# Optimization experiments

Hardware: AMD Instinct MI355X
Metric: run time of the kernel (lower is better)

## Reference

```python
import jax, jax.numpy as jnp
import numpy as np

N_NODES = 100000
N_EDGES = 1600000
IN_FEATS = 128
OUT_FEATS = 64
NUM_HEADS = 1
K_HOPS = 3
NEG_SLOPE = 0.2


def setup_inputs() -> dict:
    key = jax.random.key(0)
    kf, kw, kl, kr, ks, kd = jax.random.split(key, 6)
    feat = jax.random.normal(kf, (N_NODES, IN_FEATS), dtype=jnp.float32)
    # xavier-normal-ish scaling (gain for relu ~ sqrt(2))
    W = jax.random.normal(kw, (OUT_FEATS * NUM_HEADS, IN_FEATS), dtype=jnp.float32) * np.sqrt(2.0 / (IN_FEATS + OUT_FEATS * NUM_HEADS))
    attn_l = jax.random.normal(kl, (1, NUM_HEADS, OUT_FEATS), dtype=jnp.float32) * 0.1
    attn_r = jax.random.normal(kr, (1, NUM_HEADS, OUT_FEATS), dtype=jnp.float32) * 0.1
    src = jax.random.randint(ks, (N_EDGES,), 0, N_NODES, dtype=jnp.int32)
    dst = jax.random.randint(kd, (N_EDGES,), 0, N_NODES, dtype=jnp.int32)
    return {"feat": feat, "W": W, "attn_l": attn_l, "attn_r": attn_r, "src": src, "dst": dst}


def _edge_softmax(e, dst, n_nodes):
    # e: [E, H, 1]; softmax over incoming edges of each dst node
    emax = jax.ops.segment_max(e, dst, num_segments=n_nodes)  # [N, H, 1]
    ee = jnp.exp(e - emax[dst])
    denom = jax.ops.segment_sum(ee, dst, num_segments=n_nodes)
    return ee / denom[dst]


def reference(feat, W, attn_l, attn_r, src, dst):
    n = feat.shape[0]
    h = (feat @ W.T).reshape(n, NUM_HEADS, OUT_FEATS)  # [N, H, F]
    el = jnp.sum(h * attn_l, axis=-1, keepdims=True)   # [N, H, 1]
    er = jnp.sum(h * attn_r, axis=-1, keepdims=True)   # [N, H, 1]
    e = el[src] + er[dst]                               # [E, H, 1]
    e = jnp.where(e > 0, e, NEG_SLOPE * e)              # leaky_relu
    a = _edge_softmax(e, dst, n)                        # [E, H, 1]

    ones = jnp.ones((src.shape[0],), dtype=feat.dtype)
    out_deg = jax.ops.segment_sum(ones, src, num_segments=n)
    in_deg = jax.ops.segment_sum(ones, dst, num_segments=n)
    out_norm = jnp.power(jnp.clip(out_deg, 1.0, None), -0.5)[:, None, None]  # deg^-0.5
    in_norm = jnp.power(jnp.clip(in_deg, 1.0, None), 0.5)[:, None, None]     # deg^+0.5 (as in source)

    feat_src = h
    for _ in range(K_HOPS):
        feat_src = feat_src * out_norm
        m = feat_src[src] * a                            # [E, H, F]
        feat_src = jax.ops.segment_sum(m, dst, num_segments=n)
        feat_src = feat_src * in_norm
    return feat_src  # [N, H, F]
```

## Files before the change

kernel.cpp:

```cpp
#include <hip/hip_runtime.h>
#include <hip/hip_fp16.h>
#include <math.h>

#define N_NODES 100000
#define N_EDGES 1600000
#define IN_F 128
#define OUT_F 64
#define NEG_SLOPE 0.2f

#define NBUCK 391
#define PB 512
#define EPB (N_EDGES / PB)

#define FS 132

typedef __attribute__((ext_vector_type(8))) short short8;
typedef __attribute__((ext_vector_type(4))) float f32x4;

__device__ __forceinline__ unsigned pack_bf(float f) {
    unsigned u  = __float_as_uint(f);
    unsigned hi = u & 0xffff0000u;
    float    lo = f - __uint_as_float(hi);
    return hi | (__float_as_uint(lo) >> 16);
}

__device__ __forceinline__ void unpack8(uint4 p0, uint4 p1, short8& hi, short8& lo) {
    hi[0] = (short)(p0.x >> 16); lo[0] = (short)(p0.x & 0xffffu);
    hi[1] = (short)(p0.y >> 16); lo[1] = (short)(p0.y & 0xffffu);
    hi[2] = (short)(p0.z >> 16); lo[2] = (short)(p0.z & 0xffffu);
    hi[3] = (short)(p0.w >> 16); lo[3] = (short)(p0.w & 0xffffu);
    hi[4] = (short)(p1.x >> 16); lo[4] = (short)(p1.x & 0xffffu);
    hi[5] = (short)(p1.y >> 16); lo[5] = (short)(p1.y & 0xffffu);
    hi[6] = (short)(p1.z >> 16); lo[6] = (short)(p1.z & 0xffffu);
    hi[7] = (short)(p1.w >> 16); lo[7] = (short)(p1.w & 0xffffu);
}

__global__ __launch_bounds__(256) void k_gemm(
        const float* __restrict__ feat, const float* __restrict__ W,
        const float* __restrict__ attn_l, const float* __restrict__ attn_r,
        __half* __restrict__ h16, float* __restrict__ el, float* __restrict__ er) {
    __shared__ __align__(16) unsigned flds[64 * FS];
    __shared__ __align__(16) unsigned wlds[64 * FS];
    int t = threadIdx.x;
    int n0 = blockIdx.x * 64;

    #pragma unroll
    for (int j = 0; j < 8; ++j) {
        int idx = t + j * 256;
        int row = idx >> 5, k4 = (idx & 31) * 4;
        float4 wv = *(const float4*)&W[row * IN_F + k4];
        unsigned* wp = &wlds[row * FS + k4];
        wp[0] = pack_bf(wv.x); wp[1] = pack_bf(wv.y);
        wp[2] = pack_bf(wv.z); wp[3] = pack_bf(wv.w);
        int g = n0 + row;
        float4 fv = {0.f, 0.f, 0.f, 0.f};
        if (g < N_NODES) fv = *(const float4*)&feat[(size_t)g * IN_F + k4];
        unsigned* fp = &flds[row * FS + k4];
        fp[0] = pack_bf(fv.x); fp[1] = pack_bf(fv.y);
        fp[2] = pack_bf(fv.z); fp[3] = pack_bf(fv.w);
    }
    __syncthreads();

    int lane = t & 63, wv_ = t >> 6;
    int quad = lane >> 4, nl = lane & 15;
    int mrow = wv_ * 16 + nl;

    f32x4 acc[4];
    #pragma unroll
    for (int nt = 0; nt < 4; ++nt) acc[nt] = (f32x4){0.f, 0.f, 0.f, 0.f};

    #pragma unroll
    for (int ks = 0; ks < 4; ++ks) {
        int ko = ks * 32 + quad * 8;
        const uint4* ap = (const uint4*)&flds[mrow * FS + ko];
        uint4 a0 = ap[0], a1 = ap[1];
        short8 ahi, alo; unpack8(a0, a1, ahi, alo);
        #pragma unroll
        for (int nt = 0; nt < 4; ++nt) {
            const uint4* bp = (const uint4*)&wlds[(nt * 16 + nl) * FS + ko];
            uint4 b0 = bp[0], b1 = bp[1];
            short8 bhi, blo; unpack8(b0, b1, bhi, blo);
            acc[nt] = __builtin_amdgcn_mfma_f32_16x16x32_bf16(ahi, bhi, acc[nt], 0, 0, 0);
            acc[nt] = __builtin_amdgcn_mfma_f32_16x16x32_bf16(ahi, blo, acc[nt], 0, 0, 0);
            acc[nt] = __builtin_amdgcn_mfma_f32_16x16x32_bf16(alo, bhi, acc[nt], 0, 0, 0);
        }
    }

    float al4[4], ar4[4];
    #pragma unroll
    for (int nt = 0; nt < 4; ++nt) { al4[nt] = attn_l[nt * 16 + nl]; ar4[nt] = attn_r[nt * 16 + nl]; }
    float elp[4] = {0.f, 0.f, 0.f, 0.f}, erp[4] = {0.f, 0.f, 0.f, 0.f};
    #pragma unroll
    for (int nt = 0; nt < 4; ++nt)
        #pragma unroll
        for (int r = 0; r < 4; ++r) {
            elp[r] += acc[nt][r] * al4[nt];
            erp[r] += acc[nt][r] * ar4[nt];
        }
    #pragma unroll
    for (int off = 1; off <= 8; off <<= 1)
        #pragma unroll
        for (int r = 0; r < 4; ++r) {
            elp[r] += __shfl_xor(elp[r], off);
            erp[r] += __shfl_xor(erp[r], off);
        }
    int gbase = n0 + wv_ * 16 + quad * 4;
    if (nl == 0) {
        #pragma unroll
        for (int r = 0; r < 4; ++r) {
            int g = gbase + r;
            if (g < N_NODES) { el[g] = elp[r]; er[g] = erp[r]; }
        }
    }
    #pragma unroll
    for (int r = 0; r < 4; ++r) {
        int g = gbase + r;
        if (g < N_NODES) {
            #pragma unroll
            for (int nt = 0; nt < 4; ++nt)
                h16[(size_t)g * OUT_F + nt * 16 + nl] = __float2half(acc[nt][r]);
        }
    }
}

__global__ __launch_bounds__(256) void k_hist(
        const int* __restrict__ src, const int* __restrict__ dst,
        int* __restrict__ cntd, int* __restrict__ cnts) {
    __shared__ int hd[NBUCK], hs[NBUCK];
    int t = threadIdx.x, b = blockIdx.x;
    for (int k = t; k < NBUCK; k += 256) { hd[k] = 0; hs[k] = 0; }
    __syncthreads();
    int base = b * EPB;
    for (int i = t; i < EPB; i += 256) {
        atomicAdd(&hd[dst[base + i] >> 8], 1);
        atomicAdd(&hs[src[base + i] >> 8], 1);
    }
    __syncthreads();
    for (int k = t; k < NBUCK; k += 256) {
        cntd[k * PB + b] = hd[k];
        cnts[k * PB + b] = hs[k];
    }
}

__global__ __launch_bounds__(256) void k_colsum(const int* __restrict__ cntd,
                                                const int* __restrict__ cnts,
                                                int* __restrict__ totd,
                                                int* __restrict__ tots) {
    __shared__ int s[256];
    int b = blockIdx.x, t = threadIdx.x;
    const int* m; int* o; int k;
    if (b < NBUCK) { m = cntd; o = totd; k = b; }
    else           { m = cnts; o = tots; k = b - NBUCK; }
    s[t] = m[k * PB + t] + m[k * PB + t + 256];
    __syncthreads();
    for (int d = 128; d; d >>= 1) { if (t < d) s[t] += s[t + d]; __syncthreads(); }
    if (t == 0) o[k] = s[0];
}

__global__ __launch_bounds__(512) void k_bstart(const int* __restrict__ totd,
                                                const int* __restrict__ tots,
                                                int* bstartd, int* bstarts) {
    __shared__ int s[512];
    int t = threadIdx.x;
    int v = (t < NBUCK) ? totd[t] : 0;
    s[t] = v; __syncthreads();
    for (int d = 1; d < 512; d <<= 1) { int a = (t >= d) ? s[t - d] : 0; __syncthreads(); s[t] += a; __syncthreads(); }
    if (t <= NBUCK) bstartd[t] = s[t] - v;
    __syncthreads();
    int v2 = (t < NBUCK) ? tots[t] : 0;
    s[t] = v2; __syncthreads();
    for (int d = 1; d < 512; d <<= 1) { int a = (t >= d) ? s[t - d] : 0; __syncthreads(); s[t] += a; __syncthreads(); }
    if (t <= NBUCK) bstarts[t] = s[t] - v2;
}

__global__ __launch_bounds__(512) void k_blockoff(const int* __restrict__ bstartd,
                                                  const int* __restrict__ bstarts,
                                                  int* cntd, int* cnts) {
    __shared__ int s[512];
    int b = blockIdx.x, t = threadIdx.x;
    int* m; const int* bs; int k;
    if (b < NBUCK) { m = cntd; bs = bstartd; k = b; }
    else           { m = cnts; bs = bstarts; k = b - NBUCK; }
    int c = m[k * PB + t];
    s[t] = c; __syncthreads();
    for (int d = 1; d < 512; d <<= 1) { int a = (t >= d) ? s[t - d] : 0; __syncthreads(); s[t] += a; __syncthreads(); }
    m[k * PB + t] = bs[k] + s[t] - c;
}

__global__ __launch_bounds__(256) void k_scatter_src(
        const int* __restrict__ src, const int* __restrict__ offs,
        unsigned char* __restrict__ tmps) {
    __shared__ int lOffS[NBUCK], lFillS[NBUCK];
    int t = threadIdx.x, b = blockIdx.x;
    for (int k = t; k < NBUCK; k += 256) { lOffS[k] = offs[k * PB + b]; lFillS[k] = 0; }
    __syncthreads();
    int base = b * EPB;
    for (int i = t; i < EPB; i += 256) {
        int sN = src[base + i];
        int ks = sN >> 8;
        int rs = atomicAdd(&lFillS[ks], 1);
        tmps[lOffS[ks] + rs] = (unsigned char)(sN & 255);
    }
}

__global__ __launch_bounds__(256) void k_srccnt(
        const unsigned char* __restrict__ tmps, const int* __restrict__ bstarts,
        float* __restrict__ onorm) {
    __shared__ int cnt[256];
    int k = blockIdx.x, t = threadIdx.x;
    cnt[t] = 0; __syncthreads();
    int base = bstarts[k], end = bstarts[k + 1];
    for (int i = base + t; i < end; i += 256)
        atomicAdd(&cnt[tmps[i]], 1);
    __syncthreads();
    int idx = k * 256 + t;
    if (idx < N_NODES) onorm[idx] = rsqrtf((float)max(cnt[t], 1));
}

__global__ __launch_bounds__(256) void k_scatter3(
        const int* __restrict__ src, const int* __restrict__ dst,
        const float* __restrict__ el, const float* __restrict__ er,
        const int* __restrict__ offd, int2* __restrict__ tmpd) {
    __shared__ int lOffD[NBUCK], lFillD[NBUCK];
    int t = threadIdx.x, b = blockIdx.x;
    for (int k = t; k < NBUCK; k += 256) { lOffD[k] = offd[k * PB + b]; lFillD[k] = 0; }
    __syncthreads();
    int base = b * EPB;
    for (int i = t; i < EPB; i += 256) {
        int e = base + i;
        int sN = src[e], d = dst[e];
        float v = el[sN] + er[d];
        v = (v > 0.f) ? v : NEG_SLOPE * v;
        float pe = __expf(v);
        int kd = d >> 8;
        int rd = atomicAdd(&lFillD[kd], 1);
        int2 rec; rec.x = sN | ((d & 255) << 17); rec.y = __float_as_int(pe);
        tmpd[lOffD[kd] + rd] = rec;
    }
}

__global__ __launch_bounds__(256) void k_bucket(
        const int2* __restrict__ tmp, const int* __restrict__ bstart,
        const float* __restrict__ onorm, float2* __restrict__ csr,
        int* __restrict__ rowstart, float* __restrict__ sigma) {
    __shared__ int   cs[256];
    __shared__ int   excl[256];
    __shared__ int   fill[256];
    __shared__ float dsum[256];
    int k = blockIdx.x, t = threadIdx.x;
    int base = bstart[k], end = bstart[k + 1];
    cs[t] = 0; fill[t] = 0; dsum[t] = 0.f;
    __syncthreads();
    for (int i = base + t; i < end; i += 256)
        atomicAdd(&cs[(tmp[i].x >> 17) & 255], 1);
    __syncthreads();
    int c = cs[t];
    for (int d = 1; d < 256; d <<= 1) {
        int a = (t >= d) ? cs[t - d] : 0;
        __syncthreads();
        cs[t] += a;
        __syncthreads();
    }
    excl[t] = cs[t] - c;
    __syncthreads();
    int idx = k * 256 + t;
    if (idx <= N_NODES) rowstart[idx] = base + excl[t];
    for (int i = base + t; i < end; i += 256) {
        int2 rec = tmp[i];
        int dlow = (rec.x >> 17) & 255;
        int r = atomicAdd(&fill[dlow], 1);
        float pe = __int_as_float(rec.y);
        int sN = rec.x & 131071;
        float2 w;
        w.x = __int_as_float(sN);
        w.y = pe * onorm[sN];
        csr[base + excl[dlow] + r] = w;
        atomicAdd(&dsum[dlow], pe);
    }
    __syncthreads();
    if (idx < N_NODES) {
        float inn = sqrtf((float)max(c, 1));
        sigma[idx] = (c > 0) ? inn / dsum[t] : 0.f;
    }
}

template<typename OT>
__global__ __launch_bounds__(256) void k_spmm(
        const __half* __restrict__ x, const int* __restrict__ rowstart,
        const float2* __restrict__ csr, const float* __restrict__ sigma,
        OT* __restrict__ y) {
    int node = blockIdx.x * 16 + (threadIdx.x >> 4);
    int fl = threadIdx.x & 15;
    if (node >= N_NODES) return;
    int b = rowstart[node], e = rowstart[node + 1];
    float4 acc0 = {0.f, 0.f, 0.f, 0.f}, acc1 = {0.f, 0.f, 0.f, 0.f};
    float4 acc2 = {0.f, 0.f, 0.f, 0.f}, acc3 = {0.f, 0.f, 0.f, 0.f};
    for (int i = b; i < e; i += 8) {
        #pragma unroll
        for (int u = 0; u < 8; ++u) {
            int j = i + u;
            int jc = (j < e) ? j : (e - 1);
            float2 w = csr[jc];
            float vv = (j < e) ? w.y : 0.f;
            uint2 pk = *(const uint2*)(x + (size_t)__float_as_int(w.x) * OUT_F + fl * 4);
            float2 f0 = __half22float2(*(__half2*)&pk.x);
            float2 f1 = __half22float2(*(__half2*)&pk.y);
            float4& a = (u & 2) ? ((u & 1) ? acc3 : acc2) : ((u & 1) ? acc1 : acc0);
            a.x += vv * f0.x; a.y += vv * f0.y; a.z += vv * f1.x; a.w += vv * f1.y;
        }
    }
    float sg = sigma[node];
    float4 r;
    r.x = sg * ((acc0.x + acc1.x) + (acc2.x + acc3.x));
    r.y = sg * ((acc0.y + acc1.y) + (acc2.y + acc3.y));
    r.z = sg * ((acc0.z + acc1.z) + (acc2.z + acc3.z));
    r.w = sg * ((acc0.w + acc1.w) + (acc2.w + acc3.w));
    if constexpr (sizeof(OT) == 4) {
        ((float4*)((float*)y + (size_t)node * OUT_F))[fl] = r;
    } else {
        __half2 p0 = __floats2half2_rn(r.x, r.y);
        __half2 p1 = __floats2half2_rn(r.z, r.w);
        uint2 o;
        o.x = *(unsigned*)&p0;
        o.y = *(unsigned*)&p1;
        *(uint2*)((__half*)y + (size_t)node * OUT_F + fl * 4) = o;
    }
}

extern "C" void kernel_launch(void* const* d_in, const int* in_sizes, int n_in,
                              void* d_out, int out_size, void* d_ws, size_t ws_size,
                              hipStream_t stream) {
    const float* feat   = (const float*)d_in[0];
    const float* W      = (const float*)d_in[1];
    const float* attn_l = (const float*)d_in[2];
    const float* attn_r = (const float*)d_in[3];
    const int*   src    = (const int*)d_in[4];
    const int*   dst    = (const int*)d_in[5];
    float* out = (float*)d_out;

    char* p = (char*)d_ws;
    auto alloc = [&](size_t bytes) {
        void* r = (void*)p;
        p += (bytes + 255) & ~(size_t)255;
        return r;
    };
    __half* hbuf = (__half*)alloc((size_t)N_NODES * OUT_F * 2);
    char* r2 = (char*)alloc((size_t)N_EDGES * 8 + (size_t)N_EDGES);
    int2*  tmpd = (int2*)r2;
    unsigned char* tmps = (unsigned char*)(r2 + (size_t)N_EDGES * 8);
    __half* A   = (__half*)r2;

    float2* csr      = (float2*)alloc((size_t)N_EDGES * 8);
    int*    cntd     = (int*)   alloc((size_t)NBUCK * PB * 4);
    int*    cnts     = (int*)   alloc((size_t)NBUCK * PB * 4);
    int*    totd     = (int*)   alloc(NBUCK * 4);
    int*    tots     = (int*)   alloc(NBUCK * 4);
    int*    bstartd  = (int*)   alloc((NBUCK + 1) * 4);
    int*    bstarts  = (int*)   alloc((NBUCK + 1) * 4);
    int*    rowstart = (int*)   alloc((N_NODES + 1) * 4);
    float*  onorm    = (float*) alloc(N_NODES * 4);
    float*  sigma    = (float*) alloc(N_NODES * 4);
    float*  el       = (float*) alloc(N_NODES * 4);
    float*  er       = (float*) alloc(N_NODES * 4);

    const int NGB = (N_NODES + 63) / 64;

    k_gemm       <<<NGB,       256, 0, stream>>>(feat, W, attn_l, attn_r, hbuf, el, er);
    k_hist       <<<PB,        256, 0, stream>>>(src, dst, cntd, cnts);
    k_colsum     <<<2 * NBUCK, 256, 0, stream>>>(cntd, cnts, totd, tots);
    k_bstart     <<<1,         512, 0, stream>>>(totd, tots, bstartd, bstarts);
    k_blockoff   <<<2 * NBUCK, 512, 0, stream>>>(bstartd, bstarts, cntd, cnts);
    k_scatter_src<<<PB,        256, 0, stream>>>(src, cnts, tmps);
    k_srccnt     <<<NBUCK,     256, 0, stream>>>(tmps, bstarts, onorm);
    k_scatter3   <<<PB,        256, 0, stream>>>(src, dst, el, er, cntd, tmpd);
    k_bucket     <<<NBUCK,     256, 0, stream>>>(tmpd, bstartd, onorm, csr, rowstart, sigma);

    const int nb_spmm = N_NODES / 16;
    k_spmm<__half><<<nb_spmm, 256, 0, stream>>>(hbuf, rowstart, csr, sigma, A);
    k_spmm<__half><<<nb_spmm, 256, 0, stream>>>(A,    rowstart, csr, sigma, hbuf);
    k_spmm<float> <<<nb_spmm, 256, 0, stream>>>(hbuf, rowstart, csr, sigma, out);
}
```

Before: 321.6 us.

## Fuse src/dst scatter kernels, stage bucket CSR writes in LDS, unroll SpMM deeper

Merges the source-bucket scatter into the dst scatter kernel, so src is read once and one launch goes away. k_bucket now stages CSR records in a 5000-entry shared buffer and writes them out coalesced instead of scattering straight to global memory. The SpMM inner loop unroll goes from 8 to 16 edges to keep more gathers in flight. Trade-offs: the large LDS buffer may lower occupancy in k_bucket, and the deeper unroll wastes more masked iterations on low-degree rows.

```diff
diff --git a/kernel.cpp b/kernel.cpp
--- a/kernel.cpp
+++ b/kernel.cpp
@@ -11,6 +11,7 @@
 #define NBUCK 391
 #define PB 512
 #define EPB (N_EDGES / PB)
+#define BCAP 5000
 
 #define FS 132
 
@@ -187,43 +188,17 @@
     m[k * PB + t] = bs[k] + s[t] - c;
 }
 
-__global__ __launch_bounds__(256) void k_scatter_src(
-        const int* __restrict__ src, const int* __restrict__ offs,
-        unsigned char* __restrict__ tmps) {
-    __shared__ int lOffS[NBUCK], lFillS[NBUCK];
-    int t = threadIdx.x, b = blockIdx.x;
-    for (int k = t; k < NBUCK; k += 256) { lOffS[k] = offs[k * PB + b]; lFillS[k] = 0; }
-    __syncthreads();
-    int base = b * EPB;
-    for (int i = t; i < EPB; i += 256) {
-        int sN = src[base + i];
-        int ks = sN >> 8;
-        int rs = atomicAdd(&lFillS[ks], 1);
-        tmps[lOffS[ks] + rs] = (unsigned char)(sN & 255);
-    }
-}
-
-__global__ __launch_bounds__(256) void k_srccnt(
-        const unsigned char* __restrict__ tmps, const int* __restrict__ bstarts,
-        float* __restrict__ onorm) {
-    __shared__ int cnt[256];
-    int k = blockIdx.x, t = threadIdx.x;
-    cnt[t] = 0; __syncthreads();
-    int base = bstarts[k], end = bstarts[k + 1];
-    for (int i = base + t; i < end; i += 256)
-        atomicAdd(&cnt[tmps[i]], 1);
-    __syncthreads();
-    int idx = k * 256 + t;
-    if (idx < N_NODES) onorm[idx] = rsqrtf((float)max(cnt[t], 1));
-}
-
-__global__ __launch_bounds__(256) void k_scatter3(
+__global__ __launch_bounds__(256) void k_scatter(
         const int* __restrict__ src, const int* __restrict__ dst,
         const float* __restrict__ el, const float* __restrict__ er,
-        const int* __restrict__ offd, int2* __restrict__ tmpd) {
-    __shared__ int lOffD[NBUCK], lFillD[NBUCK];
+        const int* __restrict__ offd, const int* __restrict__ offs,
+        int2* __restrict__ tmpd, unsigned char* __restrict__ tmps) {
+    __shared__ int lOffD[NBUCK], lFillD[NBUCK], lOffS[NBUCK], lFillS[NBUCK];
     int t = threadIdx.x, b = blockIdx.x;
-    for (int k = t; k < NBUCK; k += 256) { lOffD[k] = offd[k * PB + b]; lFillD[k] = 0; }
+    for (int k = t; k < NBUCK; k += 256) {
+        lOffD[k] = offd[k * PB + b]; lFillD[k] = 0;
+        lOffS[k] = offs[k * PB + b]; lFillS[k] = 0;
+    }
     __syncthreads();
     int base = b * EPB;
     for (int i = t; i < EPB; i += 256) {
@@ -236,7 +211,24 @@
         int rd = atomicAdd(&lFillD[kd], 1);
         int2 rec; rec.x = sN | ((d & 255) << 17); rec.y = __float_as_int(pe);
         tmpd[lOffD[kd] + rd] = rec;
-    }
+        int ks = sN >> 8;
+        int rs = atomicAdd(&lFillS[ks], 1);
+        tmps[lOffS[ks] + rs] = (unsigned char)(sN & 255);
+    }
+}
+
+__global__ __launch_bounds__(256) void k_srccnt(
+        const unsigned char* __restrict__ tmps, const int* __restrict__ bstarts,
+        float* __restrict__ onorm) {
+    __shared__ int cnt[256];
+    int k = blockIdx.x, t = threadIdx.x;
+    cnt[t] = 0; __syncthreads();
+    int base = bstarts[k], end = bstarts[k + 1];
+    for (int i = base + t; i < end; i += 256)
+        atomicAdd(&cnt[tmps[i]], 1);
+    __syncthreads();
+    int idx = k * 256 + t;
+    if (idx < N_NODES) onorm[idx] = rsqrtf((float)max(cnt[t], 1));
 }
 
 __global__ __launch_bounds__(256) void k_bucket(
@@ -247,6 +239,7 @@
     __shared__ int   excl[256];
     __shared__ int   fill[256];
     __shared__ float dsum[256];
+    __shared__ float2 lbuf[BCAP];
     int k = blockIdx.x, t = threadIdx.x;
     int base = bstart[k], end = bstart[k + 1];
     cs[t] = 0; fill[t] = 0; dsum[t] = 0.f;
@@ -274,10 +267,16 @@
         float2 w;
         w.x = __int_as_float(sN);
         w.y = pe * onorm[sN];
-        csr[base + excl[dlow] + r] = w;
+        int pos = excl[dlow] + r;
+        if (pos < BCAP) lbuf[pos] = w;
+        else            csr[base + pos] = w;
         atomicAdd(&dsum[dlow], pe);
     }
     __syncthreads();
+    int n = end - base;
+    int lim = (n < BCAP) ? n : BCAP;
+    for (int q = t; q < lim; q += 256)
+        csr[base + q] = lbuf[q];
     if (idx < N_NODES) {
         float inn = sqrtf((float)max(c, 1));
         sigma[idx] = (c > 0) ? inn / dsum[t] : 0.f;
@@ -295,9 +294,9 @@
     int b = rowstart[node], e = rowstart[node + 1];
     float4 acc0 = {0.f, 0.f, 0.f, 0.f}, acc1 = {0.f, 0.f, 0.f, 0.f};
     float4 acc2 = {0.f, 0.f, 0.f, 0.f}, acc3 = {0.f, 0.f, 0.f, 0.f};
-    for (int i = b; i < e; i += 8) {
-        #pragma unroll
-        for (int u = 0; u < 8; ++u) {
+    for (int i = b; i < e; i += 16) {
+        #pragma unroll
+        for (int u = 0; u < 16; ++u) {
             int j = i + u;
             int jc = (j < e) ? j : (e - 1);
             float2 w = csr[jc];
@@ -365,15 +364,14 @@
 
     const int NGB = (N_NODES + 63) / 64;
 
-    k_gemm       <<<NGB,       256, 0, stream>>>(feat, W, attn_l, attn_r, hbuf, el, er);
-    k_hist       <<<PB,        256, 0, stream>>>(src, dst, cntd, cnts);
-    k_colsum     <<<2 * NBUCK, 256, 0, stream>>>(cntd, cnts, totd, tots);
-    k_bstart     <<<1,         512, 0, stream>>>(totd, tots, bstartd, bstarts);
-    k_blockoff   <<<2 * NBUCK, 512, 0, stream>>>(bstartd, bstarts, cntd, cnts);
-    k_scatter_src<<<PB,        256, 0, stream>>>(src, cnts, tmps);
-    k_srccnt     <<<NBUCK,     256, 0, stream>>>(tmps, bstarts, onorm);
-    k_scatter3   <<<PB,        256, 0, stream>>>(src, dst, el, er, cntd, tmpd);
-    k_bucket     <<<NBUCK,     256, 0, stream>>>(tmpd, bstartd, onorm, csr, rowstart, sigma);
+    k_gemm    <<<NGB,       256, 0, stream>>>(feat, W, attn_l, attn_r, hbuf, el, er);
+    k_hist    <<<PB,        256, 0, stream>>>(src, dst, cntd, cnts);
+    k_colsum  <<<2 * NBUCK, 256, 0, stream>>>(cntd, cnts, totd, tots);
+    k_bstart  <<<1,         512, 0, stream>>>(totd, tots, bstartd, bstarts);
+    k_blockoff<<<2 * NBUCK, 512, 0, stream>>>(bstartd, bstarts, cntd, cnts);
+    k_scatter <<<PB,        256, 0, stream>>>(src, dst, el, er, cntd, cnts, tmpd, tmps);
+    k_srccnt  <<<NBUCK,     256, 0, stream>>>(tmps, bstarts, onorm);
+    k_bucket  <<<NBUCK,     256, 0, stream>>>(tmpd, bstartd, onorm, csr, rowstart, sigma);
 
     const int nb_spmm = N_NODES / 16;
     k_spmm<__half><<<nb_spmm, 256, 0, stream>>>(hbuf, rowstart, csr, sigma, A);
```

After: 354.2 us. +10.1%, slower.
